# Performance work log

Measured on AMD Instinct MI355X. Metric: run time of the kernel, lower is better.

## Reference

```python
import jax, jax.numpy as jnp
import numpy as np
import math

K = 8       # wavelet order (k)
C = 8       # channels (c)
ALPHA = 64  # retained Fourier modes
L = 0       # coarsest level
B = 32
N = 8192    # power of two


def setup_inputs() -> dict:
    key = jax.random.key(0)
    ks = jax.random.split(key, 14)
    ck = C * K
    scale = 1.0 / (ck * ck)  # matches torch: 1/(c*k)**2
    f32 = jnp.float32
    inp = {
        "x": jax.random.normal(ks[0], (B, N, C, K), dtype=f32),
        # SparseKernelFT1d weights (complex, stored as re/im): scale * rand
        "wA_re": scale * jax.random.uniform(ks[1], (ck, ck, ALPHA), dtype=f32),
        "wA_im": scale * jax.random.uniform(ks[2], (ck, ck, ALPHA), dtype=f32),
        "wB_re": scale * jax.random.uniform(ks[3], (ck, ck, ALPHA), dtype=f32),
        "wB_im": scale * jax.random.uniform(ks[4], (ck, ck, ALPHA), dtype=f32),
        "wC_re": scale * jax.random.uniform(ks[5], (ck, ck, ALPHA), dtype=f32),
        "wC_im": scale * jax.random.uniform(ks[6], (ck, ck, ALPHA), dtype=f32),
        # T0 linear layer (k -> k)
        "T0_w": jax.random.normal(ks[7], (K, K), dtype=f32) / math.sqrt(K),
        "T0_b": 0.01 * jax.random.normal(ks[8], (K,), dtype=f32),
        # Legendre wavelet filter buffers: ec_* are [H0.T;H1.T] / [G0.T;G1.T] (2k,k),
        # rc_* are [H0;G0] / [H1;G1] (2k,k). Stand-ins: random orthonormal-ish matrices
        # scaled like wavelet filters (same math regardless of exact values).
        "ec_s": jax.random.normal(ks[9], (2 * K, K), dtype=f32) / math.sqrt(2 * K),
        "ec_d": jax.random.normal(ks[10], (2 * K, K), dtype=f32) / math.sqrt(2 * K),
        "rc_e": jax.random.normal(ks[11], (2 * K, K), dtype=f32) / math.sqrt(2 * K),
        "rc_o": jax.random.normal(ks[12], (2 * K, K), dtype=f32) / math.sqrt(2 * K),
    }
    return inp


def _sparse_ft(x, w_re, w_im):
    # x: [B, N, c, k] -> spectral mixing over first ALPHA rfft modes
    Bb, Nn, c, k = x.shape
    xv = x.reshape(Bb, Nn, c * k).transpose(0, 2, 1)   # [B, ck, N]
    xf = jnp.fft.rfft(xv)                               # [B, ck, N//2+1] complex
    l = min(ALPHA, Nn // 2 + 1)
    W = (w_re[:, :, :l] + 1j * w_im[:, :, :l]).astype(jnp.complex64)
    of = jnp.einsum('bix,iox->box', xf[:, :, :l], W)
    out_ft = jnp.zeros((Bb, c * k, Nn // 2 + 1), dtype=jnp.complex64).at[:, :, :l].set(of)
    xo = jnp.fft.irfft(out_ft, n=Nn)                    # [B, ck, N] real
    return xo.transpose(0, 2, 1).reshape(Bb, Nn, c, k)


def reference(x, wA_re, wA_im, wB_re, wB_im, wC_re, wC_im, T0_w, T0_b,
              ec_s, ec_d, rc_e, rc_o):
    Bb, Nn, c, k = x.shape
    ns = int(math.floor(math.log2(Nn)))
    Ud, Us = [], []
    # --- decomposition ---
    for _ in range(ns - L):
        xa = jnp.concatenate([x[:, ::2], x[:, 1::2]], axis=-1)  # [B, N/2, c, 2k]
        d = xa @ ec_d                                           # [B, N/2, c, k]
        s = xa @ ec_s
        Ud.append(_sparse_ft(d, wA_re, wA_im) + _sparse_ft(s, wB_re, wB_im))
        Us.append(_sparse_ft(d, wC_re, wC_im))
        x = s
    # --- coarsest-level linear ---
    x = x @ T0_w.T + T0_b
    # --- reconstruction (u_s is None branch) ---
    for i in range(ns - 1 - L, -1, -1):
        x = x + Us[i]
        xc = jnp.concatenate([x, Ud[i]], axis=-1)               # [B, n, c, 2k]
        x_e = xc @ rc_e
        x_o = xc @ rc_o
        Bc, Nc, cc, _ = xc.shape
        x = jnp.stack([x_e, x_o], axis=2).reshape(Bc, Nc * 2, cc, K)  # interleave even/odd
    return (x,) + tuple(Ud) + tuple(Us)
```

## Files before the change

### kernel.cpp

```cpp
#include <hip/hip_runtime.h>

#define BB 32
#define CKD 64
#define CC 8
#define KK 8
#define TT 64
#define FPW 132

__device__ const int D_FCB[14] = {0,32,48,56,60,62,63,64,65,66,67,68,69,70};
__device__ const int D_TB[14] = {0,64,96,112,120,124,126,127,128,129,130,131,132,133};
__device__ const int D_LS[14] = {0,64,128,192,256,320,384,417,434,443,448,451,453,454};
__device__ const int D_L[13]  = {64,64,64,64,64,64,33,17,9,5,3,2,1};
__device__ const int D_FTOF[13] = {0,524288,786432,917504,983040,1015808,1032192,
                                   1048576,1064960,1081344,1097728,1114112,1130496};

typedef __attribute__((ext_vector_type(4))) short s4v;
typedef __attribute__((ext_vector_type(8))) short s8v;
typedef __attribute__((ext_vector_type(4))) float f4v;

static __device__ __forceinline__ float4 ld4(const float* p){ return *(const float4*)p; }
static __device__ __forceinline__ size_t d_udo(int i){ return 33554432ull - (16777216u >> i); }
static __device__ __forceinline__ size_t d_uso(int i){ return 50329600ull - (16777216u >> i); }
static __device__ __forceinline__ size_t d_tof(int i){ return 128ull * (8192u - (8192u >> i)); }

static __device__ __forceinline__ unsigned short b16(float f) {
    unsigned u = __float_as_uint(f);
    u += 0x7FFFu + ((u >> 16) & 1u);
    return (unsigned short)(u >> 16);
}
static __device__ __forceinline__ float fb16(unsigned short h) {
    return __uint_as_float(((unsigned)h) << 16);
}

__global__ __launch_bounds__(256) void gen_T_k(unsigned short* __restrict__ Th,
                                               unsigned short* __restrict__ Tl) {
    int lvl = blockIdx.y;
    int nh = 4096 >> lvl;
    int idx = blockIdx.x * 256 + threadIdx.x;
    if (idx >= nh * 128) return;
    int t = idx >> 7, k = idx & 127, x = k >> 1;
    int l = nh / 2 + 1; if (l > 64) l = 64;
    float v = 0.f;
    if (x < l) {
        int r = (x * t) & (nh - 1);
        float th = 6.283185307179586f * ((float)r / (float)nh);
        float s, c; sincosf(th, &s, &c);
        v = (k & 1) ? s : c;
    }
    unsigned short hi = b16(v);
    unsigned short lo = b16(v - fb16(hi));
    size_t off = d_tof(lvl) + idx;
    Th[off] = hi; Tl[off] = lo;
}

__global__ __launch_bounds__(256) void gen_Tf_k(unsigned short* __restrict__ Tfh,
                                                unsigned short* __restrict__ Tfl) {
    int lvl = blockIdx.y;
    int nh = 4096 >> lvl;
    int nhp = nh < 128 ? 128 : nh;
    int idx = blockIdx.x * 256 + threadIdx.x;
    if (idx >= 128 * nhp) return;
    int j = idx & 7;
    int lane = (idx >> 3) & 63;
    int mt = (idx >> 9) & 7;
    int kb = idx >> 12;
    int row = mt*16 + (lane & 15);
    int t = kb*32 + (lane >> 4)*8 + j;
    int x = row >> 1;
    int l = nh / 2 + 1; if (l > 64) l = 64;
    float v = 0.f;
    if (x < l && t < nh) {
        int r = (x * t) & (nh - 1);
        float th = 6.283185307179586f * ((float)r / (float)nh);
        float s, c; sincosf(th, &s, &c);
        v = (row & 1) ? -s : c;
    }
    unsigned short hi = b16(v);
    unsigned short lo = b16(v - fb16(hi));
    size_t off = (size_t)D_FTOF[lvl] + idx;
    Tfh[off] = hi; Tfl[off] = lo;
}

__global__ __launch_bounds__(256) void decomp_k(const float* __restrict__ xin,
        const float* __restrict__ ecd, const float* __restrict__ ecs,
        float* __restrict__ dslot, float* __restrict__ sslot, int nh) {
    int idx = blockIdx.x * 256 + threadIdx.x;
    if (idx >= BB * nh * CC) return;
    int c = idx & 7;
    int t = (idx >> 3) % nh;
    int b = idx / (nh * CC);
    const float* p0 = xin + ((size_t)b * 2 * nh + 2 * t) * CKD + c * KK;
    float xa[16];
    float4 v;
    v = ld4(p0);      xa[0]=v.x; xa[1]=v.y; xa[2]=v.z; xa[3]=v.w;
    v = ld4(p0+4);    xa[4]=v.x; xa[5]=v.y; xa[6]=v.z; xa[7]=v.w;
    v = ld4(p0+64);   xa[8]=v.x; xa[9]=v.y; xa[10]=v.z; xa[11]=v.w;
    v = ld4(p0+68);   xa[12]=v.x; xa[13]=v.y; xa[14]=v.z; xa[15]=v.w;
    float dd[8], ss[8];
    #pragma unroll
    for (int m = 0; m < 8; m++) { dd[m] = 0.f; ss[m] = 0.f; }
    #pragma unroll
    for (int j = 0; j < 16; j++) {
        float xv = xa[j];
        #pragma unroll
        for (int m = 0; m < 8; m++) {
            dd[m] = fmaf(xv, ecd[j*8+m], dd[m]);
            ss[m] = fmaf(xv, ecs[j*8+m], ss[m]);
        }
    }
    size_t ob = ((size_t)b * nh + t) * CKD + c * KK;
    *(float4*)(dslot+ob)   = make_float4(dd[0],dd[1],dd[2],dd[3]);
    *(float4*)(dslot+ob+4) = make_float4(dd[4],dd[5],dd[6],dd[7]);
    *(float4*)(sslot+ob)   = make_float4(ss[0],ss[1],ss[2],ss[3]);
    *(float4*)(sslot+ob+4) = make_float4(ss[4],ss[5],ss[6],ss[7]);
}

__global__ __launch_bounds__(256) void fft_fwd_mfma_k(const float* __restrict__ outbuf,
        const unsigned short* __restrict__ Tfh, const unsigned short* __restrict__ Tfl,
        float* __restrict__ xfpf) {
    __shared__ unsigned vp[64*FPW];
    int slot = blockIdx.x;
    int lvl = 0;
    while (lvl < 12 && slot >= D_FCB[lvl+1]) lvl++;
    int nh = 4096 >> lvl;
    int t0s = (slot - D_FCB[lvl]) * 128;
    int b = blockIdx.y, z = blockIdx.z;
    const float* V = outbuf + (z ? d_uso(lvl) : d_udo(lvl)) + (size_t)b * nh * CKD;
    const unsigned short* THb = Tfh + D_FTOF[lvl];
    const unsigned short* TLb = Tfl + D_FTOF[lvl];
    int tid = threadIdx.x;
    int w = tid >> 6, lane = tid & 63;
    int col = lane & 15, khi = lane >> 4;
    int mt0 = (w & 1) * 4, nt0 = (w >> 1) * 2;
    #pragma unroll
    for (int q = 0; q < 8; q++) {
        int fi = tid + 256*q;
        int tl_ = fi >> 4;
        int t = t0s + tl_;
        int i4 = (fi & 15) * 4;
        float4 v = make_float4(0.f,0.f,0.f,0.f);
        if (t < nh) v = ld4(V + (size_t)t*CKD + i4);
        const float* pv = &v.x;
        #pragma unroll
        for (int j = 0; j < 4; j++) {
            int row = i4 + j;
            float f = pv[j];
            unsigned u = __float_as_uint(f);
            unsigned hi = u & 0xFFFF0000u;
            float r = f - __uint_as_float(hi);
            unsigned lo = __float_as_uint(r) & 0xFFFF0000u;
            int cw = tl_ ^ (((row >> 3) & 7) << 2);
            vp[row*FPW + cw] = (hi >> 16) | lo;
        }
    }
    __syncthreads();
    int rrow[2], rswz[2];
    #pragma unroll
    for (int n = 0; n < 2; n++) {
        rrow[n] = (nt0 + n)*16 + col;
        rswz[n] = ((rrow[n] >> 3) & 7) << 2;
    }
    f4v acc[4][2];
    #pragma unroll
    for (int m = 0; m < 4; m++)
        #pragma unroll
        for (int n = 0; n < 2; n++) acc[m][n] = (f4v){0.f,0.f,0.f,0.f};
    int kb0 = (slot - D_FCB[lvl]) * 4;
    #pragma unroll
    for (int kk = 0; kk < 4; kk++) {
        int kb = kb0 + kk;
        s8v ah[4], al[4];
        #pragma unroll
        for (int m = 0; m < 4; m++) {
            size_t fo = (((size_t)kb*8 + (mt0 + m))*64 + lane)*8;
            ah[m] = *(const s8v*)(THb + fo);
            al[m] = *(const s8v*)(TLb + fo);
        }
        int cb = kk*32 + khi*8;
        #pragma unroll
        for (int n = 0; n < 2; n++) {
            const unsigned* pr = vp + rrow[n]*FPW;
            uint4 w0 = *(const uint4*)(pr + (cb ^ rswz[n]));
            uint4 w1 = *(const uint4*)(pr + ((cb + 4) ^ rswz[n]));
            s8v bh, bl;
            const unsigned* pw = &w0.x;
            #pragma unroll
            for (int j = 0; j < 4; j++) {
                bh[j] = (short)(pw[j] & 0xFFFFu);
                bl[j] = (short)(pw[j] >> 16);
            }
            pw = &w1.x;
            #pragma unroll
            for (int j = 0; j < 4; j++) {
                bh[4+j] = (short)(pw[j] & 0xFFFFu);
                bl[4+j] = (short)(pw[j] >> 16);
            }
            #pragma unroll
            for (int m = 0; m < 4; m++) {
                acc[m][n] = __builtin_amdgcn_mfma_f32_16x16x32_bf16(ah[m], bh, acc[m][n], 0,0,0);
                acc[m][n] = __builtin_amdgcn_mfma_f32_16x16x32_bf16(ah[m], bl, acc[m][n], 0,0,0);
                acc[m][n] = __builtin_amdgcn_mfma_f32_16x16x32_bf16(al[m], bh, acc[m][n], 0,0,0);
            }
        }
    }
    float* P = xfpf + ((size_t)slot*64 + (size_t)b*2 + z) * 8192;
    #pragma unroll
    for (int m = 0; m < 4; m++) {
        int m0 = (mt0 + m)*16 + khi*4;
        #pragma unroll
        for (int n = 0; n < 2; n++) {
            int ic = (nt0 + n)*16 + col;
            #pragma unroll
            for (int r = 0; r < 4; r++)
                P[(size_t)(m0 + r)*64 + ic] = acc[m][n][r];
        }
    }
}

__global__ __launch_bounds__(256) void reduce_fwd_k(const float* __restrict__ xfpf,
        float2* __restrict__ xf_all) {
    int lvl = blockIdx.y;
    int e = blockIdx.x * 256 + threadIdx.x;
    int j = e & 4095;
    int bz = e >> 12;
    int x = j >> 6, i = j & 63;
    int c0 = D_FCB[lvl], c1 = D_FCB[lvl+1];
    float re = 0.f, im = 0.f;
    for (int c = c0; c < c1; c++) {
        size_t base = ((size_t)c*64 + bz) * 8192;
        re += xfpf[base + (size_t)(2*x)*64 + i];
        im += xfpf[base + (size_t)(2*x+1)*64 + i];
    }
    xf_all[(size_t)lvl*262144 + (size_t)bz*4096 + j] = make_float2(re, im);
}

__global__ __launch_bounds__(256) void mix_all_k(const float2* __restrict__ xf_all,
        const float* __restrict__ wAr, const float* __restrict__ wAi,
        const float* __restrict__ wBr, const float* __restrict__ wBi,
        const float* __restrict__ wCr, const float* __restrict__ wCi,
        unsigned short* __restrict__ ofh, unsigned short* __restrict__ ofl) {
    int lvl = 0;
    while (lvl < 12 && (int)blockIdx.x >= D_LS[lvl+1]) lvl++;
    int x = blockIdx.x - D_LS[lvl];
    int nh = 4096 >> lvl;
    const float2* xfL = xf_all + (size_t)lvl*262144;
    int tid = threadIdx.x;
    int o = tid & 63, wq = tid >> 6;
    __shared__ float2 sxd[BB*CKD];
    __shared__ float2 sxs[BB*CKD];
    __shared__ float  swt[6][16*CKD];
    for (int q = tid; q < BB*CKD; q += 256) {
        int b = q >> 6, i = q & 63;
        sxd[q] = xfL[((size_t)b*2 + 0)*4096 + x*64 + i];
        sxs[q] = xfL[((size_t)b*2 + 1)*4096 + x*64 + i];
    }
    float2 aud[8], aus[8];
    #pragma unroll
    for (int j=0;j<8;j++){ aud[j]=make_float2(0.f,0.f); aus[j]=make_float2(0.f,0.f); }
    for (int ic = 0; ic < 4; ic++) {
        __syncthreads();
        for (int q = tid; q < 16*CKD; q += 256) {
            int ii = q >> 6, oo = q & 63;
            size_t a = ((size_t)(ic*16+ii)*64 + oo)*64 + x;
            swt[0][q] = wAr[a]; swt[1][q] = wAi[a];
            swt[2][q] = wBr[a]; swt[3][q] = wBi[a];
            swt[4][q] = wCr[a]; swt[5][q] = wCi[a];
        }
        __syncthreads();
        #pragma unroll 4
        for (int ii = 0; ii < 16; ii++) {
            float ar = swt[0][ii*64+o], ai_ = swt[1][ii*64+o];
            float br = swt[2][ii*64+o], bi_ = swt[3][ii*64+o];
            float cr = swt[4][ii*64+o], ci_ = swt[5][ii*64+o];
            int i = ic*16 + ii;
            #pragma unroll
            for (int j = 0; j < 8; j++) {
                float2 xd = sxd[(wq*8+j)*64 + i];
                float2 xs = sxs[(wq*8+j)*64 + i];
                aud[j].x += xd.x*ar - xd.y*ai_ + xs.x*br - xs.y*bi_;
                aud[j].y += xd.x*ai_ + xd.y*ar + xs.x*bi_ + xs.y*br;
                aus[j].x += xd.x*cr - xd.y*ci_;
                aus[j].y += xd.x*ci_ + xd.y*cr;
            }
        }
    }
    float w = (x == 0 || 2*x == nh) ? 1.f : 2.f;
    float sc = w / (float)nh;
    int k0 = 2*x;
    #pragma unroll
    for (int j = 0; j < 8; j++) {
        int b = wq*8 + j;
        {
            size_t base = (((size_t)lvl*32 + b)*2 + 0)*8192;
            float A = sc*aud[j].x, Bn = -sc*aud[j].y;
            unsigned short ha = b16(A),  hb = b16(Bn);
            unsigned short la = b16(A - fb16(ha)), lb = b16(Bn - fb16(hb));
            ofh[base + (size_t)k0*64 + o]     = ha;
            ofh[base + (size_t)(k0+1)*64 + o] = hb;
            ofl[base + (size_t)k0*64 + o]     = la;
            ofl[base + (size_t)(k0+1)*64 + o] = lb;
        }
        {
            size_t base = (((size_t)lvl*32 + b)*2 + 1)*8192;
            float A = sc*aus[j].x, Bn = -sc*aus[j].y;
            unsigned short ha = b16(A),  hb = b16(Bn);
            unsigned short la = b16(A - fb16(ha)), lb = b16(Bn - fb16(hb));
            ofh[base + (size_t)k0*64 + o]     = ha;
            ofh[base + (size_t)(k0+1)*64 + o] = hb;
            ofl[base + (size_t)k0*64 + o]     = la;
            ofl[base + (size_t)(k0+1)*64 + o] = lb;
        }
    }
}

__global__ __launch_bounds__(256) void fft_inv_mfma_k(
        const unsigned short* __restrict__ ofh, const unsigned short* __restrict__ ofl,
        const unsigned short* __restrict__ Th,  const unsigned short* __restrict__ Tl,
        float* __restrict__ outbuf) {
    __shared__ unsigned short gh[64*132];
    __shared__ unsigned short gl[64*132];
    int lvl = 0;
    while (lvl < 12 && (int)blockIdx.x >= D_TB[lvl+1]) lvl++;
    int g = blockIdx.x - D_TB[lvl];
    int nh = 4096 >> lvl;
    int tbase = g * 64;
    int b = blockIdx.y, z = blockIdx.z;
    const unsigned short* Gh = ofh + (((size_t)lvl*32 + b)*2 + z)*8192;
    const unsigned short* Gl = ofl + (((size_t)lvl*32 + b)*2 + z)*8192;
    int tid = threadIdx.x;
    #pragma unroll
    for (int q = 0; q < 4; q++) {
        int fi = tid + 256*q;
        int k = fi & 127, oct = fi >> 7;
        uint4 vh = *(const uint4*)(Gh + (size_t)k*64 + oct*8);
        uint4 vl = *(const uint4*)(Gl + (size_t)k*64 + oct*8);
        const unsigned* ph = &vh.x;
        const unsigned* pl = &vl.x;
        #pragma unroll
        for (int i = 0; i < 8; i++) {
            unsigned wd = ph[i>>1];
            gh[(oct*8+i)*132 + k] = (i&1) ? (unsigned short)(wd>>16) : (unsigned short)(wd&0xFFFF);
            wd = pl[i>>1];
            gl[(oct*8+i)*132 + k] = (i&1) ? (unsigned short)(wd>>16) : (unsigned short)(wd&0xFFFF);
        }
    }
    __syncthreads();
    int w = tid >> 6;
    int lane = tid & 63;
    int tb = tbase + w*16;
    if (tb >= nh) return;
    int trow = lane & 15, khi = lane >> 4;
    int tA = tb + trow; if (tA >= nh) tA = nh - 1;
    const unsigned short* THp = Th + d_tof(lvl) + (size_t)tA*128 + khi*8;
    const unsigned short* TLp = Tl + d_tof(lvl) + (size_t)tA*128 + khi*8;
    f4v acc[4];
    #pragma unroll
    for (int n = 0; n < 4; n++) acc[n] = (f4v){0.f,0.f,0.f,0.f};
    #pragma unroll
    for (int kk = 0; kk < 4; kk++) {
        s8v ah = *(const s8v*)(THp + kk*32);
        s8v al = *(const s8v*)(TLp + kk*32);
        #pragma unroll
        for (int n = 0; n < 4; n++) {
            int off = (n*16 + trow)*132 + kk*32 + khi*8;
            s4v b0 = *(const s4v*)(gh + off);
            s4v b1 = *(const s4v*)(gh + off + 4);
            s4v c0 = *(const s4v*)(gl + off);
            s4v c1 = *(const s4v*)(gl + off + 4);
            s8v bh = __builtin_shufflevector(b0, b1, 0,1,2,3,4,5,6,7);
            s8v bl = __builtin_shufflevector(c0, c1, 0,1,2,3,4,5,6,7);
            acc[n] = __builtin_amdgcn_mfma_f32_16x16x32_bf16(ah, bh, acc[n], 0, 0, 0);
            acc[n] = __builtin_amdgcn_mfma_f32_16x16x32_bf16(ah, bl, acc[n], 0, 0, 0);
            acc[n] = __builtin_amdgcn_mfma_f32_16x16x32_bf16(al, bh, acc[n], 0, 0, 0);
        }
    }
    float* U = outbuf + (z ? d_uso(lvl) : d_udo(lvl)) + (size_t)b * nh * CKD;
    int thi4 = (lane >> 4) * 4;
    #pragma unroll
    for (int n = 0; n < 4; n++) {
        #pragma unroll
        for (int r = 0; r < 4; r++) {
            int t = tb + thi4 + r;
            if (t < nh) U[(size_t)t*64 + n*16 + trow] = acc[n][r];
        }
    }
}

__global__ __launch_bounds__(256) void t0_k(const float* __restrict__ xin,
        const float* __restrict__ w, const float* __restrict__ bias,
        float* __restrict__ xout) {
    int idx = blockIdx.x*256 + threadIdx.x;
    if (idx >= BB*CKD) return;
    int m = idx & 7, c = (idx >> 3) & 7, b = idx >> 6;
    const float* xr = xin + (size_t)b*CKD + c*KK;
    float acc = bias[m];
    #pragma unroll
    for (int j = 0; j < 8; j++) acc = fmaf(xr[j], w[m*8+j], acc);
    xout[idx] = acc;
}

__global__ __launch_bounds__(256) void recon_k(const float* __restrict__ xin,
        const float* __restrict__ us, const float* __restrict__ ud,
        const float* __restrict__ rce, const float* __restrict__ rco,
        float* __restrict__ xout, int nh) {
    int idx = blockIdx.x*256 + threadIdx.x;
    if (idx >= BB*nh*CC) return;
    int c = idx & 7;
    int t = (idx >> 3) % nh;
    int b = idx / (nh*CC);
    size_t base = ((size_t)b*nh + t)*CKD + c*KK;
    float xc[16];
    float4 a0 = ld4(xin+base), a1 = ld4(xin+base+4);
    float4 u0 = ld4(us+base),  u1 = ld4(us+base+4);
    float4 d0 = ld4(ud+base),  d1 = ld4(ud+base+4);
    xc[0]=a0.x+u0.x; xc[1]=a0.y+u0.y; xc[2]=a0.z+u0.z; xc[3]=a0.w+u0.w;
    xc[4]=a1.x+u1.x; xc[5]=a1.y+u1.y; xc[6]=a1.z+u1.z; xc[7]=a1.w+u1.w;
    xc[8]=d0.x;  xc[9]=d0.y;  xc[10]=d0.z; xc[11]=d0.w;
    xc[12]=d1.x; xc[13]=d1.y; xc[14]=d1.z; xc[15]=d1.w;
    float e[8], o2[8];
    #pragma unroll
    for (int m = 0; m < 8; m++) { e[m] = 0.f; o2[m] = 0.f; }
    #pragma unroll
    for (int j = 0; j < 16; j++) {
        float xv = xc[j];
        #pragma unroll
        for (int m = 0; m < 8; m++) {
            e[m]  = fmaf(xv, rce[j*8+m], e[m]);
            o2[m] = fmaf(xv, rco[j*8+m], o2[m]);
        }
    }
    size_t ob = ((size_t)b*2*nh + 2*t)*CKD + c*KK;
    *(float4*)(xout+ob)      = make_float4(e[0],e[1],e[2],e[3]);
    *(float4*)(xout+ob+4)    = make_float4(e[4],e[5],e[6],e[7]);
    *(float4*)(xout+ob+64)   = make_float4(o2[0],o2[1],o2[2],o2[3]);
    *(float4*)(xout+ob+68)   = make_float4(o2[4],o2[5],o2[6],o2[7]);
}

extern "C" void kernel_launch(void* const* d_in, const int* in_sizes, int n_in,
                              void* d_out, int out_size, void* d_ws, size_t ws_size,
                              hipStream_t stream) {
    const float* x   = (const float*)d_in[0];
    const float* wAr = (const float*)d_in[1];
    const float* wAi = (const float*)d_in[2];
    const float* wBr = (const float*)d_in[3];
    const float* wBi = (const float*)d_in[4];
    const float* wCr = (const float*)d_in[5];
    const float* wCi = (const float*)d_in[6];
    const float* T0w = (const float*)d_in[7];
    const float* T0b = (const float*)d_in[8];
    const float* ecs = (const float*)d_in[9];
    const float* ecd = (const float*)d_in[10];
    const float* rce = (const float*)d_in[11];
    const float* rco = (const float*)d_in[12];
    float* out = (float*)d_out;
    float* wsf = (float*)d_ws;

    size_t p = 0;
    float2* xf_all = (float2*)(wsf + p); p += 6815744;
    unsigned short* ofh = (unsigned short*)(wsf + p); p += 3407872;
    unsigned short* ofl = (unsigned short*)(wsf + p); p += 3407872;
    unsigned short* Th  = (unsigned short*)(wsf + p); p += 528384;
    unsigned short* Tl  = (unsigned short*)(wsf + p); p += 528384;
    unsigned short* Tfh = (unsigned short*)(wsf + p); p += 573440;
    unsigned short* Tfl = (unsigned short*)(wsf + p); p += 573440;
    float*  xt0  = wsf + p; p += 2048;
    float*  rb0  = wsf + p; p += 4194304;
    float*  rb1  = wsf + p; p += 8388608;
    float*  xfpf = wsf + p; p += 36700160;
    (void)ws_size; (void)in_sizes; (void)n_in; (void)out_size;

    size_t udo[13], uso[13];
    for (int i = 0; i < 13; i++) {
        udo[i] = 33554432ull - (16777216u >> i);
        uso[i] = 50329600ull - (16777216u >> i);
    }

    gen_T_k<<<dim3(2048, 13), 256, 0, stream>>>(Th, Tl);
    gen_Tf_k<<<dim3(2048, 13), 256, 0, stream>>>(Tfh, Tfl);

    for (int i = 0; i < 13; i++) {
        int nh = 4096 >> i;
        const float* xin_l = (i == 0) ? x : (out + uso[i-1]);
        int tot = BB * nh * CC;
        decomp_k<<<(tot + 255)/256, 256, 0, stream>>>(xin_l, ecd, ecs, out + udo[i], out + uso[i], nh);
    }
    t0_k<<<(BB*CKD + 255)/256, 256, 0, stream>>>(out + uso[12], T0w, T0b, xt0);

    fft_fwd_mfma_k<<<dim3(70, BB, 2), 256, 0, stream>>>(out, Tfh, Tfl, xfpf);
    reduce_fwd_k<<<dim3(1024, 13), 256, 0, stream>>>(xfpf, xf_all);
    mix_all_k<<<454, 256, 0, stream>>>(xf_all, wAr, wAi, wBr, wBi, wCr, wCi, ofh, ofl);
    fft_inv_mfma_k<<<dim3(133, BB, 2), 256, 0, stream>>>(ofh, ofl, Th, Tl, out);

    const float* rin = xt0;
    for (int i = 12; i >= 0; i--) {
        int nh = 4096 >> i;
        float* ro = (i == 0) ? out : ((i & 1) ? rb1 : rb0);
        int tot = BB * nh * CC;
        recon_k<<<(tot + 255)/256, 256, 0, stream>>>(rin, out + uso[i], out + udo[i], rce, rco, ro, nh);
        rin = ro;
    }
}
```

Baseline: 492.9 us.

## Fuse small-level decomposition and reconstruction into single per-batch kernels

```diff
diff --git a/kernel.cpp b/kernel.cpp
--- a/kernel.cpp
+++ b/kernel.cpp
@@ -115,14 +115,71 @@
     *(float4*)(sslot+ob+4) = make_float4(ss[4],ss[5],ss[6],ss[7]);
 }
 
+__global__ __launch_bounds__(256) void decomp_small_k(const float* __restrict__ s4base,
+        const float* __restrict__ ecd, const float* __restrict__ ecs,
+        const float* __restrict__ T0w, const float* __restrict__ T0b,
+        float* __restrict__ outbuf, float* __restrict__ xt0) {
+    __shared__ float sA[128*64];
+    __shared__ float sB[64*64];
+    int b = blockIdx.x, tid = threadIdx.x;
+    for (int lvl = 5; lvl <= 12; lvl++) {
+        int nh = 4096 >> lvl;
+        const float* src = (lvl == 5) ? (s4base + (size_t)b*256*CKD)
+                                      : (((lvl - 6) & 1) ? sB : sA);
+        float* dst = ((lvl - 5) & 1) ? sB : sA;
+        float* dG = outbuf + d_udo(lvl) + (size_t)b*nh*CKD;
+        float* sG = outbuf + d_uso(lvl) + (size_t)b*nh*CKD;
+        for (int q = tid; q < nh*8; q += 256) {
+            int c = q & 7, t = q >> 3;
+            const float* p0 = src + (size_t)(2*t)*CKD + c*KK;
+            float xa[16];
+            float4 v;
+            v = ld4(p0);      xa[0]=v.x; xa[1]=v.y; xa[2]=v.z; xa[3]=v.w;
+            v = ld4(p0+4);    xa[4]=v.x; xa[5]=v.y; xa[6]=v.z; xa[7]=v.w;
+            v = ld4(p0+64);   xa[8]=v.x; xa[9]=v.y; xa[10]=v.z; xa[11]=v.w;
+            v = ld4(p0+68);   xa[12]=v.x; xa[13]=v.y; xa[14]=v.z; xa[15]=v.w;
+            float dd[8], ss[8];
+            #pragma unroll
+            for (int m = 0; m < 8; m++) { dd[m] = 0.f; ss[m] = 0.f; }
+            #pragma unroll
+            for (int j = 0; j < 16; j++) {
+                float xv = xa[j];
+                #pragma unroll
+                for (int m = 0; m < 8; m++) {
+                    dd[m] = fmaf(xv, ecd[j*8+m], dd[m]);
+                    ss[m] = fmaf(xv, ecs[j*8+m], ss[m]);
+                }
+            }
+            size_t ob = (size_t)t * CKD + c * KK;
+            *(float4*)(dG+ob)   = make_float4(dd[0],dd[1],dd[2],dd[3]);
+            *(float4*)(dG+ob+4) = make_float4(dd[4],dd[5],dd[6],dd[7]);
+            *(float4*)(sG+ob)   = make_float4(ss[0],ss[1],ss[2],ss[3]);
+            *(float4*)(sG+ob+4) = make_float4(ss[4],ss[5],ss[6],ss[7]);
+            float* dl = dst + t*CKD + c*KK;
+            #pragma unroll
+            for (int j = 0; j < 8; j++) dl[j] = ss[j];
+        }
+        __syncthreads();
+    }
+    if (tid < 64) {
+        int m = tid & 7, c = tid >> 3;
+        const float* xr = sB + c*KK;
+        float a = T0b[m];
+        #pragma unroll
+        for (int j = 0; j < 8; j++) a = fmaf(xr[j], T0w[m*8+j], a);
+        xt0[(size_t)b*64 + tid] = a;
+    }
+}
+
 __global__ __launch_bounds__(256) void fft_fwd_mfma_k(const float* __restrict__ outbuf,
         const unsigned short* __restrict__ Tfh, const unsigned short* __restrict__ Tfl,
-        float* __restrict__ xfpf) {
+        float* __restrict__ xfpf, float2* __restrict__ xf_all) {
     __shared__ unsigned vp[64*FPW];
     int slot = blockIdx.x;
     int lvl = 0;
     while (lvl < 12 && slot >= D_FCB[lvl+1]) lvl++;
     int nh = 4096 >> lvl;
+    int ch = D_FCB[lvl+1] - D_FCB[lvl];
     int t0s = (slot - D_FCB[lvl]) * 128;
     int b = blockIdx.y, z = blockIdx.z;
     const float* V = outbuf + (z ? d_uso(lvl) : d_udo(lvl)) + (size_t)b * nh * CKD;
@@ -203,16 +260,33 @@
             }
         }
     }
-    float* P = xfpf + ((size_t)slot*64 + (size_t)b*2 + z) * 8192;
-    #pragma unroll
-    for (int m = 0; m < 4; m++) {
-        int m0 = (mt0 + m)*16 + khi*4;
-        #pragma unroll
-        for (int n = 0; n < 2; n++) {
-            int ic = (nt0 + n)*16 + col;
-            #pragma unroll
-            for (int r = 0; r < 4; r++)
-                P[(size_t)(m0 + r)*64 + ic] = acc[m][n][r];
+    if (ch == 1) {
+        float* X = (float*)xf_all + ((size_t)lvl*262144 + ((size_t)b*2 + z)*4096)*2;
+        #pragma unroll
+        for (int m = 0; m < 4; m++) {
+            int m0 = (mt0 + m)*16 + khi*4;
+            #pragma unroll
+            for (int n = 0; n < 2; n++) {
+                int ic = (nt0 + n)*16 + col;
+                #pragma unroll
+                for (int r = 0; r < 4; r++) {
+                    int row = m0 + r;
+                    X[(((size_t)(row >> 1)*64 + ic) << 1) | (row & 1)] = acc[m][n][r];
+                }
+            }
+        }
+    } else {
+        float* P = xfpf + ((size_t)slot*64 + (size_t)b*2 + z) * 8192;
+        #pragma unroll
+        for (int m = 0; m < 4; m++) {
+            int m0 = (mt0 + m)*16 + khi*4;
+            #pragma unroll
+            for (int n = 0; n < 2; n++) {
+                int ic = (nt0 + n)*16 + col;
+                #pragma unroll
+                for (int r = 0; r < 4; r++)
+                    P[(size_t)(m0 + r)*64 + ic] = acc[m][n][r];
+            }
         }
     }
 }
@@ -386,17 +460,58 @@
     }
 }
 
-__global__ __launch_bounds__(256) void t0_k(const float* __restrict__ xin,
-        const float* __restrict__ w, const float* __restrict__ bias,
-        float* __restrict__ xout) {
-    int idx = blockIdx.x*256 + threadIdx.x;
-    if (idx >= BB*CKD) return;
-    int m = idx & 7, c = (idx >> 3) & 7, b = idx >> 6;
-    const float* xr = xin + (size_t)b*CKD + c*KK;
-    float acc = bias[m];
-    #pragma unroll
-    for (int j = 0; j < 8; j++) acc = fmaf(xr[j], w[m*8+j], acc);
-    xout[idx] = acc;
+__global__ __launch_bounds__(256) void recon_small_k(const float* __restrict__ xt0,
+        const float* __restrict__ outbuf,
+        const float* __restrict__ rce, const float* __restrict__ rco,
+        float* __restrict__ rb0) {
+    __shared__ float xA[128*64];
+    __shared__ float xB[64*64];
+    int b = blockIdx.x, tid = threadIdx.x;
+    if (tid < 64) xB[tid] = xt0[(size_t)b*64 + tid];
+    __syncthreads();
+    for (int i = 12; i >= 6; i--) {
+        int nh = 4096 >> i;
+        const float* cur = ((i == 12) || !(i & 1)) ? xB : xA;
+        float* nxt = (i & 1) ? xB : xA;
+        const float* Us = outbuf + d_uso(i) + (size_t)b*nh*CKD;
+        const float* Ud = outbuf + d_udo(i) + (size_t)b*nh*CKD;
+        for (int q = tid; q < nh*8; q += 256) {
+            int c = q & 7, t = q >> 3;
+            size_t base = (size_t)t*CKD + c*KK;
+            float xc[16];
+            float4 a0 = ld4(cur+base), a1 = ld4(cur+base+4);
+            float4 u0 = ld4(Us+base),  u1 = ld4(Us+base+4);
+            float4 d0 = ld4(Ud+base),  d1 = ld4(Ud+base+4);
+            xc[0]=a0.x+u0.x; xc[1]=a0.y+u0.y; xc[2]=a0.z+u0.z; xc[3]=a0.w+u0.w;
+            xc[4]=a1.x+u1.x; xc[5]=a1.y+u1.y; xc[6]=a1.z+u1.z; xc[7]=a1.w+u1.w;
+            xc[8]=d0.x;  xc[9]=d0.y;  xc[10]=d0.z; xc[11]=d0.w;
+            xc[12]=d1.x; xc[13]=d1.y; xc[14]=d1.z; xc[15]=d1.w;
+            float e[8], o2[8];
+            #pragma unroll
+            for (int m = 0; m < 8; m++) { e[m] = 0.f; o2[m] = 0.f; }
+            #pragma unroll
+            for (int j = 0; j < 16; j++) {
+                float xv = xc[j];
+                #pragma unroll
+                for (int m = 0; m < 8; m++) {
+                    e[m]  = fmaf(xv, rce[j*8+m], e[m]);
+                    o2[m] = fmaf(xv, rco[j*8+m], o2[m]);
+                }
+            }
+            if (i > 6) {
+                float* pe = nxt + (size_t)(2*t)*CKD + c*KK;
+                #pragma unroll
+                for (int j = 0; j < 8; j++) { pe[j] = e[j]; pe[CKD + j] = o2[j]; }
+            } else {
+                float* pe = rb0 + ((size_t)b*128 + 2*t)*CKD + c*KK;
+                *(float4*)(pe)      = make_float4(e[0],e[1],e[2],e[3]);
+                *(float4*)(pe+4)    = make_float4(e[4],e[5],e[6],e[7]);
+                *(float4*)(pe+64)   = make_float4(o2[0],o2[1],o2[2],o2[3]);
+                *(float4*)(pe+68)   = make_float4(o2[4],o2[5],o2[6],o2[7]);
+            }
+        }
+        __syncthreads();
+    }
 }
 
 __global__ __launch_bounds__(256) void recon_k(const float* __restrict__ xin,
@@ -478,21 +593,22 @@
     gen_T_k<<<dim3(2048, 13), 256, 0, stream>>>(Th, Tl);
     gen_Tf_k<<<dim3(2048, 13), 256, 0, stream>>>(Tfh, Tfl);
 
-    for (int i = 0; i < 13; i++) {
+    for (int i = 0; i < 5; i++) {
         int nh = 4096 >> i;
         const float* xin_l = (i == 0) ? x : (out + uso[i-1]);
         int tot = BB * nh * CC;
         decomp_k<<<(tot + 255)/256, 256, 0, stream>>>(xin_l, ecd, ecs, out + udo[i], out + uso[i], nh);
     }
-    t0_k<<<(BB*CKD + 255)/256, 256, 0, stream>>>(out + uso[12], T0w, T0b, xt0);
-
-    fft_fwd_mfma_k<<<dim3(70, BB, 2), 256, 0, stream>>>(out, Tfh, Tfl, xfpf);
-    reduce_fwd_k<<<dim3(1024, 13), 256, 0, stream>>>(xfpf, xf_all);
+    decomp_small_k<<<BB, 256, 0, stream>>>(out + uso[4], ecd, ecs, T0w, T0b, out, xt0);
+
+    fft_fwd_mfma_k<<<dim3(70, BB, 2), 256, 0, stream>>>(out, Tfh, Tfl, xfpf, xf_all);
+    reduce_fwd_k<<<dim3(1024, 5), 256, 0, stream>>>(xfpf, xf_all);
     mix_all_k<<<454, 256, 0, stream>>>(xf_all, wAr, wAi, wBr, wBi, wCr, wCi, ofh, ofl);
     fft_inv_mfma_k<<<dim3(133, BB, 2), 256, 0, stream>>>(ofh, ofl, Th, Tl, out);
 
-    const float* rin = xt0;
-    for (int i = 12; i >= 0; i--) {
+    recon_small_k<<<BB, 256, 0, stream>>>(xt0, out, rce, rco, rb0);
+    const float* rin = rb0;
+    for (int i = 5; i >= 0; i--) {
         int nh = 4096 >> i;
         float* ro = (i == 0) ? out : ((i & 1) ? rb1 : rb0);
         int tot = BB * nh * CC;
```

After: 489.7 us. Within noise of the previous version (-0.7%).
